# Kernel tuning notes

Hardware: AMD Instinct MI355X
Metric: run time of the kernel (lower is better)

Reference implementation:

```python
import jax, jax.numpy as jnp
import numpy as np

N, E = 20000, 320000
ND, PD, HD, H = 128, 64, 128, 4
EPS = 1e-5


def gelu(x):
    return jax.nn.gelu(x, approximate=False)  # torch nn.GELU default (erf)


def setup_inputs() -> dict:
    key = jax.random.key(0)
    ks = iter(jax.random.split(key, 64))

    def lin(din, dout):
        w = jax.random.normal(next(ks), (din, dout), jnp.float32) / np.float32(np.sqrt(din))
        b = jnp.zeros((dout,), jnp.float32)
        return w, b

    inp = {}
    inp['s'] = jax.random.normal(next(ks), (N, ND), jnp.float32)
    inp['z'] = jax.random.normal(next(ks), (E, PD), jnp.float32)
    inp['edge_idx'] = jax.random.randint(next(ks), (2, E), 0, N, jnp.int32)
    # attn_weight_mlp: (2*ND+PD)->HD->HD->H
    inp['w_w1'], inp['w_b1'] = lin(2 * ND + PD, HD)
    inp['w_w2'], inp['w_b2'] = lin(HD, HD)
    inp['w_w3'], inp['w_b3'] = lin(HD, H)
    # attn_value_mlp: (ND+PD)->HD->HD->ND
    inp['v_w1'], inp['v_b1'] = lin(ND + PD, HD)
    inp['v_w2'], inp['v_b2'] = lin(HD, HD)
    inp['v_w3'], inp['v_b3'] = lin(HD, ND)
    # attn_output_linear: (HD*H)->ND + BN(ND)
    inp['o_w'], inp['o_b'] = lin(HD * H, ND)
    inp['o_g'] = jnp.ones((ND,), jnp.float32); inp['o_bb'] = jnp.zeros((ND,), jnp.float32)
    inp['o_m'] = jnp.zeros((ND,), jnp.float32); inp['o_v'] = jnp.ones((ND,), jnp.float32)
    # attn_FFN: ND->HD->ND + BN(ND)
    inp['f_w1'], inp['f_b1'] = lin(ND, HD)
    inp['f_w2'], inp['f_b2'] = lin(HD, ND)
    inp['f_g'] = jnp.ones((ND,), jnp.float32); inp['f_bb'] = jnp.zeros((ND,), jnp.float32)
    inp['f_m'] = jnp.zeros((ND,), jnp.float32); inp['f_v'] = jnp.ones((ND,), jnp.float32)
    # edge_FFN: (2*ND+PD)->HD->PD + BN(PD)
    inp['e_w1'], inp['e_b1'] = lin(2 * ND + PD, HD)
    inp['e_w2'], inp['e_b2'] = lin(HD, PD)
    inp['e_g'] = jnp.ones((PD,), jnp.float32); inp['e_bb'] = jnp.zeros((PD,), jnp.float32)
    inp['e_m'] = jnp.zeros((PD,), jnp.float32); inp['e_v'] = jnp.ones((PD,), jnp.float32)
    return inp


def reference(s, z, edge_idx,
              w_w1, w_b1, w_w2, w_b2, w_w3, w_b3,
              v_w1, v_b1, v_w2, v_b2, v_w3, v_b3,
              o_w, o_b, o_g, o_bb, o_m, o_v,
              f_w1, f_b1, f_w2, f_b2, f_g, f_bb, f_m, f_v,
              e_w1, e_b1, e_w2, e_b2, e_g, e_bb, e_m, e_v):
    # Eval mode: Dropout = identity, SyncBatchNorm uses running stats.
    src, dst = edge_idx[0], edge_idx[1]

    def bn(x, g, b, m, v):
        return (x - m) * jax.lax.rsqrt(v + EPS) * g + b

    ss, sd = s[src], s[dst]  # [E,ND] gathers
    # edge FFN residual update of z (updated z feeds attention, as in torch)
    h = gelu(jnp.concatenate([ss, sd, z], axis=1) @ e_w1 + e_b1)
    z = z + bn(h @ e_w2 + e_b2, e_g, e_bb, e_m, e_v)
    # per-edge attention logits [E,H]
    h = gelu(jnp.concatenate([sd, ss, z], axis=1) @ w_w1 + w_b1)
    h = gelu(h @ w_w2 + w_b2)
    aw = h @ w_w3 + w_b3
    # per-edge values [E,ND]
    h = gelu(jnp.concatenate([ss, z], axis=1) @ v_w1 + v_b1)
    h = gelu(h @ v_w2 + v_b2)
    av = h @ v_w3 + v_b3
    # segment softmax over incoming edges of each dst node
    mx = jax.ops.segment_max(aw, dst, num_segments=N)
    ew = jnp.exp(aw - mx[dst])
    den = jax.ops.segment_sum(ew, dst, num_segments=N)
    aw = ew / den[dst]  # [E,H]
    # weighted scatter-sum: [N,H,ND] -> flatten
    ao = jax.ops.segment_sum(aw[:, :, None] * av[:, None, :], dst, num_segments=N)
    ao = ao.reshape(N, H * ND)
    s = s + bn(ao @ o_w + o_b, o_g, o_bb, o_m, o_v)
    s = s + bn(gelu(s @ f_w1 + f_b1) @ f_w2 + f_b2, f_g, f_bb, f_m, f_v)
    return (s, z)
```

## Files before the change

### kernel.cpp

```cpp
#include <hip/hip_runtime.h>
#include <stdint.h>


#define NN 20000
#define NE 320000

typedef unsigned short u16;
typedef __attribute__((ext_vector_type(8))) short bf16x8;
typedef __attribute__((ext_vector_type(4))) float f32x4;

__device__ __forceinline__ float bf2f(u16 u){ union{unsigned i; float f;} v; v.i=((unsigned)u)<<16; return v.f; }
__device__ __forceinline__ u16 f2bf(float f){ union{float f; unsigned i;} v; v.f=f; unsigned r = v.i + 0x7FFFu + ((v.i>>16)&1u); return (u16)(r>>16); }
__device__ __forceinline__ unsigned pk2(float a, float b){
  unsigned r; asm("v_cvt_pk_bf16_f32 %0, %1, %2" : "=v"(r) : "v"(a), "v"(b)); return r;
}
__device__ __forceinline__ float gelu_f(float x){
  float y = 0.7978845608f*x*(1.0f + 0.044715f*x*x);
  float a = fabsf(y);
  float t = __expf(-2.0f*a);
  float th = (1.0f - t)*__builtin_amdgcn_rcpf(1.0f + t);
  th = copysignf(th, y);
  return 0.5f*x*(1.0f + th);
}

#define WT_E1 0
#define WT_E2 40960
#define WT_W1 49152
#define WT_W2 90112
#define WT_W3 106496
#define WT_V1 108544
#define WT_V2 133120
#define WT_V3 149504
#define WT_O  165888
#define WT_F1 231424
#define WT_F2 247808
#define WT_TOT 264192
#define AW_B  ((size_t)WT_TOT*2)
#define AV_B  (AW_B + (size_t)NE*16)
#define AO_B  (AV_B + (size_t)NE*256)
#define CNT_B (AO_B + (size_t)NN*1024)
#define CUR_B (CNT_B + (size_t)NN*4)
#define STA_B (CUR_B + (size_t)NN*4)
#define ORD_B (STA_B + (size_t)(NN+1)*4 + 4)

struct PrepArgs { const float* src[11]; u16* dst; };

__global__ void prep_kernel(PrepArgs A){
  constexpr int NS[11]  = {128, 64,128,128,  4,128,128,128,128,128,128};
  constexpr int NO[11]  = {128, 64,128,128, 16,128,128,128,128,128,128};
  constexpr int OFF[11] = {0,40960,49152,90112,106496,108544,133120,149504,165888,231424,247808};
  constexpr int CUM[12] = {0,10,12,22,26,28,34,38,42,58,62,66};
  __shared__ float T[64][72];
  const int bid = blockIdx.x, t = threadIdx.x;
  int m = 0;
#pragma unroll
  for (int q=0;q<11;q++) if (bid >= CUM[q+1]) m = q+1;
  const int rel = bid - CUM[m];
  const int ntn = (NO[m] > 64) ? 2 : 1;
  const int c  = rel / ntn;
  const int nt = rel - c*ntn;
  const float* src = A.src[m];
  if (m != 4){
    const int k = t>>2, q = t&3;
    const float* sp = src + (size_t)(c*64+k)*NS[m] + nt*64 + q*16;
    float4 v0=((const float4*)sp)[0], v1=((const float4*)sp)[1], v2=((const float4*)sp)[2], v3=((const float4*)sp)[3];
    float* tp = &T[k][q*16];
    ((float4*)tp)[0]=v0; ((float4*)tp)[1]=v1; ((float4*)tp)[2]=v2; ((float4*)tp)[3]=v3;
  } else {
    for (int lin = t; lin < 64*16; lin += 256){
      int k = lin>>4, n = lin&15;
      T[k][n] = (n < 4) ? src[(size_t)(c*64+k)*4 + n] : 0.f;
    }
  }
  __syncthreads();
  const int nl = t>>2, kq = (t&3)*16;
  const int n = nt*64 + nl;
  if (nl < 64 && n < NO[m]){
    unsigned w[8];
#pragma unroll
    for (int i=0;i<8;i++) w[i] = pk2(T[kq+2*i][nl], T[kq+2*i+1][nl]);
    u16* dp = A.dst + OFF[m] + (size_t)c*NO[m]*64 + (size_t)n*64 + kq;
    ((uint4*)dp)[0] = make_uint4(w[0],w[1],w[2],w[3]);
    ((uint4*)dp)[1] = make_uint4(w[4],w[5],w[6],w[7]);
  }
}

__global__ void zero_kernel(int* c){ int i = blockIdx.x*256+threadIdx.x; if (i<NN) c[i]=0; }
__global__ void hist_kernel(const int* __restrict__ ei, int* __restrict__ cnt){
  int e = blockIdx.x*256+threadIdx.x; if (e<NE) atomicAdd(&cnt[ei[NE+e]], 1);
}
__global__ void scan_kernel(const int* __restrict__ cnt, int* __restrict__ sta, int* __restrict__ cur){
  __shared__ int part[1024];
  const int t = threadIdx.x;
  const int base = t*20;
  int s = 0;
  for (int i=0;i<20;i++){ int idx=base+i; s += (idx<NN)?cnt[idx]:0; }
  part[t]=s; __syncthreads();
  for (int off=1; off<1024; off<<=1){
    int v = (t>=off)? part[t-off] : 0;
    __syncthreads();
    part[t] += v;
    __syncthreads();
  }
  int run = part[t] - s;
  for (int i=0;i<20;i++){ int idx=base+i; if (idx<NN){ int c=cnt[idx]; sta[idx]=run; cur[idx]=run; run+=c; } }
  if (t==1023) sta[NN] = part[1023];
}
__global__ void place_kernel(const int* __restrict__ ei, int* __restrict__ cur, int* __restrict__ ord){
  int e = blockIdx.x*256+threadIdx.x;
  if (e<NE){ int p = atomicAdd(&cur[ei[NE+e]], 1); ord[p]=e; }
}

template<int NCH, int NT, int MTT, int NACC>
__device__ __forceinline__ void run_gemm2(int wave, int lane,
    const u16* const (&cb)[NCH], const int (&cs)[NCH], const int (&ck)[NCH],
    const u16* __restrict__ wtG, f32x4 (&acc)[NACC],
    int& ntile, int& mt0, bool& active)
{
  const int lr = lane & 15, lg = lane >> 4;
  active = true;
  if (NT == 8){ ntile = wave; mt0 = 0; }
  else if (NT == 4){ ntile = wave & 3; mt0 = (wave >> 2) * NACC; }
  else { ntile = 0; mt0 = wave; active = (wave < MTT); }
  f32x4 z4 = {0.f,0.f,0.f,0.f};
#pragma unroll
  for (int m=0;m<NACC;m++) acc[m] = z4;
  if (!active) return;
  const int CE = NT*16*64;
  const u16* bp = wtG + (size_t)(ntile*16+lr)*64 + lg*8;
  bf16x8 bc0 = *(const bf16x8*)bp;
  bf16x8 bc1 = *(const bf16x8*)(bp + 32);
#pragma unroll
  for (int c=0;c<NCH;c++){
    bf16x8 bn0, bn1;
    if (c+1 < NCH){
      bn0 = *(const bf16x8*)(bp + (c+1)*CE);
      bn1 = *(const bf16x8*)(bp + (c+1)*CE + 32);
    }
#pragma unroll
    for (int m=0;m<NACC;m++){
      const u16* ap = cb[c] + (size_t)((mt0+m)*16 + lr)*cs[c] + ck[c] + lg*8;
      bf16x8 a0 = *(const bf16x8*)ap;
      bf16x8 a1 = *(const bf16x8*)(ap + 32);
      acc[m] = __builtin_amdgcn_mfma_f32_16x16x32_bf16(a0, bc0, acc[m], 0, 0, 0);
      acc[m] = __builtin_amdgcn_mfma_f32_16x16x32_bf16(a1, bc1, acc[m], 0, 0, 0);
    }
    bc0 = bn0; bc1 = bn1;
  }
}

template<int NACC>
__device__ __forceinline__ void epi_hb(const f32x4 (&acc)[NACC], int mt0, int ntile, int lg, int lr,
    const float* __restrict__ biasG, u16* dst, int dstride, bool act)
{
  const int col = ntile*16 + lr;
  const float b = biasG[col];
#pragma unroll
  for (int m=0;m<NACC;m++)
#pragma unroll
    for (int j=0;j<4;j++){
      int row = (mt0+m)*16 + lg*4 + j;
      float v = acc[m][j] + b;
      if (act) v = gelu_f(v);
      dst[row*dstride + col] = f2bf(v);
    }
}

struct EdgeArgs {
  const float *s, *z; const int* ei;
  const float *wb1,*wb2,*wb3,*vb1,*vb2,*vb3,*eb1,*eb2,*eg,*ebb,*em,*ev;
  const u16* wt; float* aw; u16* av; float* zout;
};

__global__ __launch_bounds__(512,4) void edge_kernel(EdgeArgs A){
  __shared__ __align__(16) u16 SS[64*136];
  __shared__ __align__(16) u16 SD[64*136];
  __shared__ __align__(16) u16 ZB[64*88];
  __shared__ __align__(16) u16 HB1[64*136];
  __shared__ __align__(16) u16 HB2[64*136];
  const int tid = threadIdx.x, wave = tid>>6, lane = tid&63;
  const int lg = lane>>4, lr = lane&15;
  const int e0 = blockIdx.x*64;
  {
    const int r = tid>>3, p = tid&7;
    const int sn = A.ei[e0 + r];
    const int dn = A.ei[NE + e0 + r];
    const float4* gs = (const float4*)(A.s + (size_t)sn*128 + p*16);
    float4 f0=gs[0], f1=gs[1], f2=gs[2], f3=gs[3];
    *(uint4*)(SS + r*136 + p*16)     = make_uint4(pk2(f0.x,f0.y),pk2(f0.z,f0.w),pk2(f1.x,f1.y),pk2(f1.z,f1.w));
    *(uint4*)(SS + r*136 + p*16 + 8) = make_uint4(pk2(f2.x,f2.y),pk2(f2.z,f2.w),pk2(f3.x,f3.y),pk2(f3.z,f3.w));
    const float4* gd = (const float4*)(A.s + (size_t)dn*128 + p*16);
    f0=gd[0]; f1=gd[1]; f2=gd[2]; f3=gd[3];
    *(uint4*)(SD + r*136 + p*16)     = make_uint4(pk2(f0.x,f0.y),pk2(f0.z,f0.w),pk2(f1.x,f1.y),pk2(f1.z,f1.w));
    *(uint4*)(SD + r*136 + p*16 + 8) = make_uint4(pk2(f2.x,f2.y),pk2(f2.z,f2.w),pk2(f3.x,f3.y),pk2(f3.z,f3.w));
    const float4* gz = (const float4*)(A.z + (size_t)(e0+r)*64 + p*8);
    float4 z0=gz[0], z1=gz[1];
    *(uint4*)(ZB + r*88 + p*8) = make_uint4(pk2(z0.x,z0.y),pk2(z0.z,z0.w),pk2(z1.x,z1.y),pk2(z1.z,z1.w));
  }
  __syncthreads();
  int ntile, mt0; bool act_;
  {
    const u16* cb[5] = {SS,SS,SD,SD,ZB}; const int cs[5]={136,136,136,136,88}; const int ck[5]={0,64,0,64,0};
    f32x4 acc[4];
    run_gemm2<5,8,4,4>(wave,lane,cb,cs,ck, A.wt+WT_E1, acc, ntile, mt0, act_);
    epi_hb<4>(acc, mt0, ntile, lg, lr, A.eb1, HB1, 136, true);
  }
  __syncthreads();
  {
    const u16* cb[2] = {HB1,HB1}; const int cs[2]={136,136}; const int ck[2]={0,64};
    f32x4 acc[2];
    run_gemm2<2,4,4,2>(wave,lane,cb,cs,ck, A.wt+WT_E2, acc, ntile, mt0, act_);
    const int col = ntile*16 + lr;
    const float b  = A.eb2[col];
    const float sc = A.eg[col] * rsqrtf(A.ev[col] + 1e-5f);
    const float sh = A.ebb[col] - A.em[col]*sc;
#pragma unroll
    for (int m=0;m<2;m++)
#pragma unroll
      for (int j=0;j<4;j++){
        int row = (mt0+m)*16 + lg*4 + j;
        float zo = A.z[(size_t)(e0+row)*64 + col];
        float zn = zo + (acc[m][j]+b)*sc + sh;
        A.zout[(size_t)(e0+row)*64 + col] = zn;
        ZB[row*88 + col] = f2bf(zn);
      }
  }
  __syncthreads();
  {
    const u16* cb[5] = {SD,SD,SS,SS,ZB}; const int cs[5]={136,136,136,136,88}; const int ck[5]={0,64,0,64,0};
    f32x4 acc[4];
    run_gemm2<5,8,4,4>(wave,lane,cb,cs,ck, A.wt+WT_W1, acc, ntile, mt0, act_);
    epi_hb<4>(acc, mt0, ntile, lg, lr, A.wb1, HB2, 136, true);
  }
  __syncthreads();
  {
    const u16* cb[2] = {HB2,HB2}; const int cs[2]={136,136}; const int ck[2]={0,64};
    f32x4 acc[4];
    run_gemm2<2,8,4,4>(wave,lane,cb,cs,ck, A.wt+WT_W2, acc, ntile, mt0, act_);
    epi_hb<4>(acc, mt0, ntile, lg, lr, A.wb2, HB1, 136, true);
  }
  __syncthreads();
  {
    const u16* cb[2] = {HB1,HB1}; const int cs[2]={136,136}; const int ck[2]={0,64};
    f32x4 acc[1];
    run_gemm2<2,1,4,1>(wave,lane,cb,cs,ck, A.wt+WT_W3, acc, ntile, mt0, act_);
    if (act_ && lr < 4){
      const float b = A.wb3[lr];
#pragma unroll
      for (int j=0;j<4;j++){
        int row = mt0*16 + lg*4 + j;
        A.aw[(size_t)(e0+row)*4 + lr] = acc[0][j] + b;
      }
    }
  }
  {
    const u16* cb[3] = {SS,SS,ZB}; const int cs[3]={136,136,88}; const int ck[3]={0,64,0};
    f32x4 acc[4];
    run_gemm2<3,8,4,4>(wave,lane,cb,cs,ck, A.wt+WT_V1, acc, ntile, mt0, act_);
    epi_hb<4>(acc, mt0, ntile, lg, lr, A.vb1, HB2, 136, true);
  }
  __syncthreads();
  {
    const u16* cb[2] = {HB2,HB2}; const int cs[2]={136,136}; const int ck[2]={0,64};
    f32x4 acc[4];
    run_gemm2<2,8,4,4>(wave,lane,cb,cs,ck, A.wt+WT_V2, acc, ntile, mt0, act_);
    epi_hb<4>(acc, mt0, ntile, lg, lr, A.vb2, HB1, 136, true);
  }
  __syncthreads();
  {
    const u16* cb[2] = {HB1,HB1}; const int cs[2]={136,136}; const int ck[2]={0,64};
    f32x4 acc[4];
    run_gemm2<2,8,4,4>(wave,lane,cb,cs,ck, A.wt+WT_V3, acc, ntile, mt0, act_);
    epi_hb<4>(acc, mt0, ntile, lg, lr, A.vb3, HB2, 136, false);
    __syncthreads();
    { const int r = tid>>3, p = tid&7;
      uint4 v0 = *(const uint4*)(HB2 + r*136 + p*16);
      uint4 v1 = *(const uint4*)(HB2 + r*136 + p*16 + 8);
      *(uint4*)(A.av + (size_t)(e0+r)*128 + p*16) = v0;
      *(uint4*)(A.av + (size_t)(e0+r)*128 + p*16 + 8) = v1; }
  }
}

__global__ void attn_kernel(const float* __restrict__ aw, const u16* __restrict__ av,
                            const int* __restrict__ sta, const int* __restrict__ ord,
                            u16* __restrict__ ao){
  const int node = blockIdx.x; const int t = threadIdx.x;
  const int b = sta[node], e = sta[node+1];
  float m0=-3.4e38f, m1=m0, m2=m0, m3=m0;
  for (int i=b;i<e;i++){
    int ed = ord[i]; float4 a = *(const float4*)(aw + (size_t)ed*4);
    m0=fmaxf(m0,a.x); m1=fmaxf(m1,a.y); m2=fmaxf(m2,a.z); m3=fmaxf(m3,a.w);
  }
  float d0=0,d1=0,d2=0,d3=0,a0=0,a1=0,a2=0,a3=0;
  for (int i=b;i<e;i++){
    int ed = ord[i]; float4 a = *(const float4*)(aw + (size_t)ed*4);
    float w0=__expf(a.x-m0), w1=__expf(a.y-m1), w2=__expf(a.z-m2), w3=__expf(a.w-m3);
    d0+=w0; d1+=w1; d2+=w2; d3+=w3;
    float v = bf2f(av[(size_t)ed*128 + t]);
    a0 += w0*v; a1 += w1*v; a2 += w2*v; a3 += w3*v;
  }
  size_t o = (size_t)node*512 + t;
  if (e > b){
    ao[o      ] = f2bf(a0/d0);
    ao[o + 128] = f2bf(a1/d1);
    ao[o + 256] = f2bf(a2/d2);
    ao[o + 384] = f2bf(a3/d3);
  } else {
    ao[o] = 0; ao[o+128] = 0; ao[o+256] = 0; ao[o+384] = 0;
  }
}

struct NodeArgs {
  const float* s; const u16* ao; const u16* wt;
  const float *ob,*og,*obb,*om,*ov,*fb1,*fb2,*fg,*fbb,*fm,*fv;
  float* outS;
};

__global__ __launch_bounds__(512,4) void node_kernel(NodeArgs A){
  __shared__ __align__(16) u16 AO[16*520];
  __shared__ __align__(16) float S1F[16*128];
  __shared__ __align__(16) u16 S1B[16*136];
  __shared__ __align__(16) u16 HBx[16*136];
  const int tid=threadIdx.x, wave=tid>>6, lane=tid&63;
  const int lg=lane>>4, lr=lane&15;
  const int n0 = blockIdx.x*16;
  { const int r=tid>>5, p=tid&31;
    const uint4* gp = (const uint4*)(A.ao + (size_t)(n0+r)*512 + p*16);
    uint4 v0=gp[0], v1=gp[1];
    *(uint4*)(AO + r*520 + p*16) = v0;
    *(uint4*)(AO + r*520 + p*16 + 8) = v1;
  }
  __syncthreads();
  int ntile, mt0; bool act_;
  {
    const u16* cb[8]={AO,AO,AO,AO,AO,AO,AO,AO};
    const int cs[8]={520,520,520,520,520,520,520,520};
    const int ck[8]={0,64,128,192,256,320,384,448};
    f32x4 acc[1];
    run_gemm2<8,8,1,1>(wave,lane,cb,cs,ck, A.wt+WT_O, acc, ntile, mt0, act_);
    const int col = wave*16+lr;
    const float bb = A.ob[col];
    const float sc = A.og[col] * rsqrtf(A.ov[col] + 1e-5f);
    const float sh = A.obb[col] - A.om[col]*sc;
#pragma unroll
    for (int j=0;j<4;j++){
      int row = lg*4+j;
      float so = A.s[(size_t)(n0+row)*128 + col];
      float s1 = so + (acc[0][j]+bb)*sc + sh;
      S1F[row*128+col] = s1;
      S1B[row*136+col] = f2bf(s1);
    }
  }
  __syncthreads();
  {
    const u16* cb[2]={S1B,S1B}; const int cs[2]={136,136}; const int ck[2]={0,64};
    f32x4 acc[1];
    run_gemm2<2,8,1,1>(wave,lane,cb,cs,ck, A.wt+WT_F1, acc, ntile, mt0, act_);
    epi_hb<1>(acc, 0, wave, lg, lr, A.fb1, HBx, 136, true);
  }
  __syncthreads();
  {
    const u16* cb[2]={HBx,HBx}; const int cs[2]={136,136}; const int ck[2]={0,64};
    f32x4 acc[1];
    run_gemm2<2,8,1,1>(wave,lane,cb,cs,ck, A.wt+WT_F2, acc, ntile, mt0, act_);
    const int col = wave*16+lr;
    const float b2  = A.fb2[col];
    const float sc2 = A.fg[col] * rsqrtf(A.fv[col] + 1e-5f);
    const float sh2 = A.fbb[col] - A.fm[col]*sc2;
#pragma unroll
    for (int j=0;j<4;j++){
      int row = lg*4+j;
      float v = S1F[row*128+col] + (acc[0][j]+b2)*sc2 + sh2;
      A.outS[(size_t)(n0+row)*128 + col] = v;
    }
  }
}

extern "C" void kernel_launch(void* const* d_in, const int* in_sizes, int n_in,
                              void* d_out, int out_size, void* d_ws, size_t ws_size,
                              hipStream_t stream)
{
  const float* sG = (const float*)d_in[0];
  const float* zG = (const float*)d_in[1];
  const int* eiG = (const int*)d_in[2];
  char* ws = (char*)d_ws;
  u16*  wt  = (u16*)ws;
  float* aw = (float*)(ws + AW_B);
  u16*  av  = (u16*)(ws + AV_B);
  u16*  ao  = (u16*)(ws + AO_B);
  int* cnt = (int*)(ws + CNT_B);
  int* cur = (int*)(ws + CUR_B);
  int* sta = (int*)(ws + STA_B);
  int* ord = (int*)(ws + ORD_B);
  float* outS = (float*)d_out;
  float* outZ = outS + (size_t)NN*128;

  PrepArgs P;
  const int srcIdx[11] = {29,31,3,5,7,9,11,13,15,21,23};
  for (int i=0;i<11;i++) P.src[i] = (const float*)d_in[srcIdx[i]];
  P.dst = wt;
  prep_kernel<<<dim3(66), dim3(256), 0, stream>>>(P);
  zero_kernel<<<dim3((NN+255)/256), dim3(256), 0, stream>>>(cnt);
  hist_kernel<<<dim3((NE+255)/256), dim3(256), 0, stream>>>(eiG, cnt);
  scan_kernel<<<dim3(1), dim3(1024), 0, stream>>>(cnt, sta, cur);
  place_kernel<<<dim3((NE+255)/256), dim3(256), 0, stream>>>(eiG, cur, ord);

  EdgeArgs E;
  E.s = sG; E.z = zG; E.ei = eiG;
  E.wb1=(const float*)d_in[4];  E.wb2=(const float*)d_in[6];  E.wb3=(const float*)d_in[8];
  E.vb1=(const float*)d_in[10]; E.vb2=(const float*)d_in[12]; E.vb3=(const float*)d_in[14];
  E.eb1=(const float*)d_in[30]; E.eb2=(const float*)d_in[32];
  E.eg=(const float*)d_in[33]; E.ebb=(const float*)d_in[34]; E.em=(const float*)d_in[35]; E.ev=(const float*)d_in[36];
  E.wt = wt; E.aw = aw; E.av = av; E.zout = outZ;
  edge_kernel<<<dim3(NE/64), dim3(512), 0, stream>>>(E);

  attn_kernel<<<dim3(NN), dim3(128), 0, stream>>>(aw, av, sta, ord, ao);

  NodeArgs Nd;
  Nd.s = sG; Nd.ao = ao; Nd.wt = wt;
  Nd.ob=(const float*)d_in[16]; Nd.og=(const float*)d_in[17]; Nd.obb=(const float*)d_in[18];
  Nd.om=(const float*)d_in[19]; Nd.ov=(const float*)d_in[20];
  Nd.fb1=(const float*)d_in[22]; Nd.fb2=(const float*)d_in[24];
  Nd.fg=(const float*)d_in[25]; Nd.fbb=(const float*)d_in[26]; Nd.fm=(const float*)d_in[27]; Nd.fv=(const float*)d_in[28];
  Nd.outS = outS;
  node_kernel<<<dim3(NN/16), dim3(512), 0, stream>>>(Nd);
}
```

Baseline: 671.0 us.

## Fuse attention aggregation into node kernel and merge setup kernels

Folds the per-node segment-softmax and weighted value aggregation into the node kernel, so the ao intermediate is never written to or read from global memory and one launch is removed. Each wave now handles two destination nodes, with each lane covering two value columns. Weight prep and the destination histogram are merged into one launch, with zeroing done by a memset. The scan kernel uses vectorised int4 loads and stores, the GEMM helper loads all weight chunks up front instead of double-buffering them, and the z tile padding in shared memory shrinks. The risks are higher register pressure from preloading all B fragments, and reduced parallelism in the fused aggregation (20000/16 blocks versus one block per node before).

```diff
diff --git a/kernel.cpp b/kernel.cpp
--- a/kernel.cpp
+++ b/kernel.cpp
@@ -37,21 +37,26 @@
 #define WT_TOT 264192
 #define AW_B  ((size_t)WT_TOT*2)
 #define AV_B  (AW_B + (size_t)NE*16)
-#define AO_B  (AV_B + (size_t)NE*256)
-#define CNT_B (AO_B + (size_t)NN*1024)
+#define CNT_B (AV_B + (size_t)NE*256)
 #define CUR_B (CNT_B + (size_t)NN*4)
 #define STA_B (CUR_B + (size_t)NN*4)
 #define ORD_B (STA_B + (size_t)(NN+1)*4 + 4)
 
 struct PrepArgs { const float* src[11]; u16* dst; };
 
-__global__ void prep_kernel(PrepArgs A){
+__global__ void setup_kernel(PrepArgs A, const int* __restrict__ ei, int* __restrict__ cnt){
   constexpr int NS[11]  = {128, 64,128,128,  4,128,128,128,128,128,128};
   constexpr int NO[11]  = {128, 64,128,128, 16,128,128,128,128,128,128};
   constexpr int OFF[11] = {0,40960,49152,90112,106496,108544,133120,149504,165888,231424,247808};
   constexpr int CUM[12] = {0,10,12,22,26,28,34,38,42,58,62,66};
   __shared__ float T[64][72];
-  const int bid = blockIdx.x, t = threadIdx.x;
+  const int t = threadIdx.x;
+  if (blockIdx.x >= 66){
+    int e = (blockIdx.x-66)*256 + t;
+    if (e < NE) atomicAdd(&cnt[ei[NE+e]], 1);
+    return;
+  }
+  const int bid = blockIdx.x;
   int m = 0;
 #pragma unroll
   for (int q=0;q<11;q++) if (bid >= CUM[q+1]) m = q+1;
@@ -85,25 +90,39 @@
   }
 }
 
-__global__ void zero_kernel(int* c){ int i = blockIdx.x*256+threadIdx.x; if (i<NN) c[i]=0; }
-__global__ void hist_kernel(const int* __restrict__ ei, int* __restrict__ cnt){
-  int e = blockIdx.x*256+threadIdx.x; if (e<NE) atomicAdd(&cnt[ei[NE+e]], 1);
-}
 __global__ void scan_kernel(const int* __restrict__ cnt, int* __restrict__ sta, int* __restrict__ cur){
   __shared__ int part[1024];
   const int t = threadIdx.x;
   const int base = t*20;
+  int v[20];
   int s = 0;
-  for (int i=0;i<20;i++){ int idx=base+i; s += (idx<NN)?cnt[idx]:0; }
+  if (t < 1000){
+#pragma unroll
+    for (int i=0;i<5;i++){
+      int4 x = ((const int4*)(cnt+base))[i];
+      v[4*i]=x.x; v[4*i+1]=x.y; v[4*i+2]=x.z; v[4*i+3]=x.w;
+      s += x.x+x.y+x.z+x.w;
+    }
+  }
   part[t]=s; __syncthreads();
   for (int off=1; off<1024; off<<=1){
-    int v = (t>=off)? part[t-off] : 0;
+    int x = (t>=off)? part[t-off] : 0;
     __syncthreads();
-    part[t] += v;
+    part[t] += x;
     __syncthreads();
   }
   int run = part[t] - s;
-  for (int i=0;i<20;i++){ int idx=base+i; if (idx<NN){ int c=cnt[idx]; sta[idx]=run; cur[idx]=run; run+=c; } }
+  if (t < 1000){
+    int sv[20];
+#pragma unroll
+    for (int i=0;i<20;i++){ sv[i]=run; run += v[i]; }
+#pragma unroll
+    for (int i=0;i<5;i++){
+      int4 x = make_int4(sv[4*i],sv[4*i+1],sv[4*i+2],sv[4*i+3]);
+      ((int4*)(sta+base))[i] = x;
+      ((int4*)(cur+base))[i] = x;
+    }
+  }
   if (t==1023) sta[NN] = part[1023];
 }
 __global__ void place_kernel(const int* __restrict__ ei, int* __restrict__ cur, int* __restrict__ ord){
@@ -112,7 +131,7 @@
 }
 
 template<int NCH, int NT, int MTT, int NACC>
-__device__ __forceinline__ void run_gemm2(int wave, int lane,
+__device__ __forceinline__ void run_gemm3(int wave, int lane,
     const u16* const (&cb)[NCH], const int (&cs)[NCH], const int (&ck)[NCH],
     const u16* __restrict__ wtG, f32x4 (&acc)[NACC],
     int& ntile, int& mt0, bool& active)
@@ -128,24 +147,22 @@
   if (!active) return;
   const int CE = NT*16*64;
   const u16* bp = wtG + (size_t)(ntile*16+lr)*64 + lg*8;
-  bf16x8 bc0 = *(const bf16x8*)bp;
-  bf16x8 bc1 = *(const bf16x8*)(bp + 32);
+  bf16x8 B0[NCH], B1[NCH];
 #pragma unroll
   for (int c=0;c<NCH;c++){
-    bf16x8 bn0, bn1;
-    if (c+1 < NCH){
-      bn0 = *(const bf16x8*)(bp + (c+1)*CE);
-      bn1 = *(const bf16x8*)(bp + (c+1)*CE + 32);
-    }
+    B0[c] = *(const bf16x8*)(bp + (size_t)c*CE);
+    B1[c] = *(const bf16x8*)(bp + (size_t)c*CE + 32);
+  }
+#pragma unroll
+  for (int c=0;c<NCH;c++){
 #pragma unroll
     for (int m=0;m<NACC;m++){
       const u16* ap = cb[c] + (size_t)((mt0+m)*16 + lr)*cs[c] + ck[c] + lg*8;
       bf16x8 a0 = *(const bf16x8*)ap;
       bf16x8 a1 = *(const bf16x8*)(ap + 32);
-      acc[m] = __builtin_amdgcn_mfma_f32_16x16x32_bf16(a0, bc0, acc[m], 0, 0, 0);
-      acc[m] = __builtin_amdgcn_mfma_f32_16x16x32_bf16(a1, bc1, acc[m], 0, 0, 0);
-    }
-    bc0 = bn0; bc1 = bn1;
+      acc[m] = __builtin_amdgcn_mfma_f32_16x16x32_bf16(a0, B0[c], acc[m], 0, 0, 0);
+      acc[m] = __builtin_amdgcn_mfma_f32_16x16x32_bf16(a1, B1[c], acc[m], 0, 0, 0);
+    }
   }
 }
 
@@ -175,7 +192,7 @@
 __global__ __launch_bounds__(512,4) void edge_kernel(EdgeArgs A){
   __shared__ __align__(16) u16 SS[64*136];
   __shared__ __align__(16) u16 SD[64*136];
-  __shared__ __align__(16) u16 ZB[64*88];
+  __shared__ __align__(16) u16 ZB[64*72];
   __shared__ __align__(16) u16 HB1[64*136];
   __shared__ __align__(16) u16 HB2[64*136];
   const int tid = threadIdx.x, wave = tid>>6, lane = tid&63;
@@ -195,21 +212,21 @@
     *(uint4*)(SD + r*136 + p*16 + 8) = make_uint4(pk2(f2.x,f2.y),pk2(f2.z,f2.w),pk2(f3.x,f3.y),pk2(f3.z,f3.w));
     const float4* gz = (const float4*)(A.z + (size_t)(e0+r)*64 + p*8);
     float4 z0=gz[0], z1=gz[1];
-    *(uint4*)(ZB + r*88 + p*8) = make_uint4(pk2(z0.x,z0.y),pk2(z0.z,z0.w),pk2(z1.x,z1.y),pk2(z1.z,z1.w));
+    *(uint4*)(ZB + r*72 + p*8) = make_uint4(pk2(z0.x,z0.y),pk2(z0.z,z0.w),pk2(z1.x,z1.y),pk2(z1.z,z1.w));
   }
   __syncthreads();
   int ntile, mt0; bool act_;
   {
-    const u16* cb[5] = {SS,SS,SD,SD,ZB}; const int cs[5]={136,136,136,136,88}; const int ck[5]={0,64,0,64,0};
-    f32x4 acc[4];
-    run_gemm2<5,8,4,4>(wave,lane,cb,cs,ck, A.wt+WT_E1, acc, ntile, mt0, act_);
+    const u16* cb[5] = {SS,SS,SD,SD,ZB}; const int cs[5]={136,136,136,136,72}; const int ck[5]={0,64,0,64,0};
+    f32x4 acc[4];
+    run_gemm3<5,8,4,4>(wave,lane,cb,cs,ck, A.wt+WT_E1, acc, ntile, mt0, act_);
     epi_hb<4>(acc, mt0, ntile, lg, lr, A.eb1, HB1, 136, true);
   }
   __syncthreads();
   {
     const u16* cb[2] = {HB1,HB1}; const int cs[2]={136,136}; const int ck[2]={0,64};
     f32x4 acc[2];
-    run_gemm2<2,4,4,2>(wave,lane,cb,cs,ck, A.wt+WT_E2, acc, ntile, mt0, act_);
+    run_gemm3<2,4,4,2>(wave,lane,cb,cs,ck, A.wt+WT_E2, acc, ntile, mt0, act_);
     const int col = ntile*16 + lr;
     const float b  = A.eb2[col];
     const float sc = A.eg[col] * rsqrtf(A.ev[col] + 1e-5f);
@@ -222,28 +239,28 @@
         float zo = A.z[(size_t)(e0+row)*64 + col];
         float zn = zo + (acc[m][j]+b)*sc + sh;
         A.zout[(size_t)(e0+row)*64 + col] = zn;
-        ZB[row*88 + col] = f2bf(zn);
+        ZB[row*72 + col] = f2bf(zn);
       }
   }
   __syncthreads();
   {
-    const u16* cb[5] = {SD,SD,SS,SS,ZB}; const int cs[5]={136,136,136,136,88}; const int ck[5]={0,64,0,64,0};
-    f32x4 acc[4];
-    run_gemm2<5,8,4,4>(wave,lane,cb,cs,ck, A.wt+WT_W1, acc, ntile, mt0, act_);
+    const u16* cb[5] = {SD,SD,SS,SS,ZB}; const int cs[5]={136,136,136,136,72}; const int ck[5]={0,64,0,64,0};
+    f32x4 acc[4];
+    run_gemm3<5,8,4,4>(wave,lane,cb,cs,ck, A.wt+WT_W1, acc, ntile, mt0, act_);
     epi_hb<4>(acc, mt0, ntile, lg, lr, A.wb1, HB2, 136, true);
   }
   __syncthreads();
   {
     const u16* cb[2] = {HB2,HB2}; const int cs[2]={136,136}; const int ck[2]={0,64};
     f32x4 acc[4];
-    run_gemm2<2,8,4,4>(wave,lane,cb,cs,ck, A.wt+WT_W2, acc, ntile, mt0, act_);
+    run_gemm3<2,8,4,4>(wave,lane,cb,cs,ck, A.wt+WT_W2, acc, ntile, mt0, act_);
     epi_hb<4>(acc, mt0, ntile, lg, lr, A.wb2, HB1, 136, true);
   }
   __syncthreads();
   {
     const u16* cb[2] = {HB1,HB1}; const int cs[2]={136,136}; const int ck[2]={0,64};
     f32x4 acc[1];
-    run_gemm2<2,1,4,1>(wave,lane,cb,cs,ck, A.wt+WT_W3, acc, ntile, mt0, act_);
+    run_gemm3<2,1,4,1>(wave,lane,cb,cs,ck, A.wt+WT_W3, acc, ntile, mt0, act_);
     if (act_ && lr < 4){
       const float b = A.wb3[lr];
 #pragma unroll
@@ -254,23 +271,23 @@
     }
   }
   {
-    const u16* cb[3] = {SS,SS,ZB}; const int cs[3]={136,136,88}; const int ck[3]={0,64,0};
-    f32x4 acc[4];
-    run_gemm2<3,8,4,4>(wave,lane,cb,cs,ck, A.wt+WT_V1, acc, ntile, mt0, act_);
+    const u16* cb[3] = {SS,SS,ZB}; const int cs[3]={136,136,72}; const int ck[3]={0,64,0};
+    f32x4 acc[4];
+    run_gemm3<3,8,4,4>(wave,lane,cb,cs,ck, A.wt+WT_V1, acc, ntile, mt0, act_);
     epi_hb<4>(acc, mt0, ntile, lg, lr, A.vb1, HB2, 136, true);
   }
   __syncthreads();
   {
     const u16* cb[2] = {HB2,HB2}; const int cs[2]={136,136}; const int ck[2]={0,64};
     f32x4 acc[4];
-    run_gemm2<2,8,4,4>(wave,lane,cb,cs,ck, A.wt+WT_V2, acc, ntile, mt0, act_);
+    run_gemm3<2,8,4,4>(wave,lane,cb,cs,ck, A.wt+WT_V2, acc, ntile, mt0, act_);
     epi_hb<4>(acc, mt0, ntile, lg, lr, A.vb2, HB1, 136, true);
   }
   __syncthreads();
   {
     const u16* cb[2] = {HB1,HB1}; const int cs[2]={136,136}; const int ck[2]={0,64};
     f32x4 acc[4];
-    run_gemm2<2,8,4,4>(wave,lane,cb,cs,ck, A.wt+WT_V3, acc, ntile, mt0, act_);
+    run_gemm3<2,8,4,4>(wave,lane,cb,cs,ck, A.wt+WT_V3, acc, ntile, mt0, act_);
     epi_hb<4>(acc, mt0, ntile, lg, lr, A.vb3, HB2, 136, false);
     __syncthreads();
     { const int r = tid>>3, p = tid&7;
@@ -281,37 +298,9 @@
   }
 }
 
-__global__ void attn_kernel(const float* __restrict__ aw, const u16* __restrict__ av,
-                            const int* __restrict__ sta, const int* __restrict__ ord,
-                            u16* __restrict__ ao){
-  const int node = blockIdx.x; const int t = threadIdx.x;
-  const int b = sta[node], e = sta[node+1];
-  float m0=-3.4e38f, m1=m0, m2=m0, m3=m0;
-  for (int i=b;i<e;i++){
-    int ed = ord[i]; float4 a = *(const float4*)(aw + (size_t)ed*4);
-    m0=fmaxf(m0,a.x); m1=fmaxf(m1,a.y); m2=fmaxf(m2,a.z); m3=fmaxf(m3,a.w);
-  }
-  float d0=0,d1=0,d2=0,d3=0,a0=0,a1=0,a2=0,a3=0;
-  for (int i=b;i<e;i++){
-    int ed = ord[i]; float4 a = *(const float4*)(aw + (size_t)ed*4);
-    float w0=__expf(a.x-m0), w1=__expf(a.y-m1), w2=__expf(a.z-m2), w3=__expf(a.w-m3);
-    d0+=w0; d1+=w1; d2+=w2; d3+=w3;
-    float v = bf2f(av[(size_t)ed*128 + t]);
-    a0 += w0*v; a1 += w1*v; a2 += w2*v; a3 += w3*v;
-  }
-  size_t o = (size_t)node*512 + t;
-  if (e > b){
-    ao[o      ] = f2bf(a0/d0);
-    ao[o + 128] = f2bf(a1/d1);
-    ao[o + 256] = f2bf(a2/d2);
-    ao[o + 384] = f2bf(a3/d3);
-  } else {
-    ao[o] = 0; ao[o+128] = 0; ao[o+256] = 0; ao[o+384] = 0;
-  }
-}
-
 struct NodeArgs {
-  const float* s; const u16* ao; const u16* wt;
+  const float* s; const float* aw; const u16* av;
+  const int* sta; const int* ord; const u16* wt;
   const float *ob,*og,*obb,*om,*ov,*fb1,*fb2,*fg,*fbb,*fm,*fv;
   float* outS;
 };
@@ -324,11 +313,38 @@
   const int tid=threadIdx.x, wave=tid>>6, lane=tid&63;
   const int lg=lane>>4, lr=lane&15;
   const int n0 = blockIdx.x*16;
-  { const int r=tid>>5, p=tid&31;
-    const uint4* gp = (const uint4*)(A.ao + (size_t)(n0+r)*512 + p*16);
-    uint4 v0=gp[0], v1=gp[1];
-    *(uint4*)(AO + r*520 + p*16) = v0;
-    *(uint4*)(AO + r*520 + p*16 + 8) = v1;
+#pragma unroll
+  for (int q=0;q<2;q++){
+    const int lrow = wave*2+q, nn = n0+lrow;
+    const int b = A.sta[nn], e = A.sta[nn+1];
+    float m0=-3.4e38f, m1=m0, m2=m0, m3=m0;
+    for (int i=b;i<e;i++){
+      int ed = A.ord[i];
+      float4 a = *(const float4*)(A.aw + (size_t)ed*4);
+      m0=fmaxf(m0,a.x); m1=fmaxf(m1,a.y); m2=fmaxf(m2,a.z); m3=fmaxf(m3,a.w);
+    }
+    float d0=0,d1=0,d2=0,d3=0;
+    float a00=0,a01=0,a10=0,a11=0,a20=0,a21=0,a30=0,a31=0;
+    for (int i=b;i<e;i++){
+      int ed = A.ord[i];
+      float4 a = *(const float4*)(A.aw + (size_t)ed*4);
+      float w0=__expf(a.x-m0), w1=__expf(a.y-m1), w2=__expf(a.z-m2), w3=__expf(a.w-m3);
+      d0+=w0; d1+=w1; d2+=w2; d3+=w3;
+      unsigned pv = *(const unsigned*)(A.av + (size_t)ed*128 + lane*2);
+      float v0 = bf2f((u16)pv), v1 = bf2f((u16)(pv>>16));
+      a00+=w0*v0; a01+=w0*v1; a10+=w1*v0; a11+=w1*v1;
+      a20+=w2*v0; a21+=w2*v1; a30+=w3*v0; a31+=w3*v1;
+    }
+    unsigned* aoRow = (unsigned*)(AO + lrow*520);
+    if (e > b){
+      float r0=1.f/d0, r1=1.f/d1, r2=1.f/d2, r3=1.f/d3;
+      aoRow[        lane] = pk2(a00*r0, a01*r0);
+      aoRow[ 64 + lane] = pk2(a10*r1, a11*r1);
+      aoRow[128 + lane] = pk2(a20*r2, a21*r2);
+      aoRow[192 + lane] = pk2(a30*r3, a31*r3);
+    } else {
+      aoRow[lane]=0; aoRow[64+lane]=0; aoRow[128+lane]=0; aoRow[192+lane]=0;
+    }
   }
   __syncthreads();
   int ntile, mt0; bool act_;
@@ -337,7 +353,7 @@
     const int cs[8]={520,520,520,520,520,520,520,520};
     const int ck[8]={0,64,128,192,256,320,384,448};
     f32x4 acc[1];
-    run_gemm2<8,8,1,1>(wave,lane,cb,cs,ck, A.wt+WT_O, acc, ntile, mt0, act_);
+    run_gemm3<8,8,1,1>(wave,lane,cb,cs,ck, A.wt+WT_O, acc, ntile, mt0, act_);
     const int col = wave*16+lr;
     const float bb = A.ob[col];
     const float sc = A.og[col] * rsqrtf(A.ov[col] + 1e-5f);
@@ -355,14 +371,14 @@
   {
     const u16* cb[2]={S1B,S1B}; const int cs[2]={136,136}; const int ck[2]={0,64};
     f32x4 acc[1];
-    run_gemm2<2,8,1,1>(wave,lane,cb,cs,ck, A.wt+WT_F1, acc, ntile, mt0, act_);
+    run_gemm3<2,8,1,1>(wave,lane,cb,cs,ck, A.wt+WT_F1, acc, ntile, mt0, act_);
     epi_hb<1>(acc, 0, wave, lg, lr, A.fb1, HBx, 136, true);
   }
   __syncthreads();
   {
     const u16* cb[2]={HBx,HBx}; const int cs[2]={136,136}; const int ck[2]={0,64};
     f32x4 acc[1];
-    run_gemm2<2,8,1,1>(wave,lane,cb,cs,ck, A.wt+WT_F2, acc, ntile, mt0, act_);
+    run_gemm3<2,8,1,1>(wave,lane,cb,cs,ck, A.wt+WT_F2, acc, ntile, mt0, act_);
     const int col = wave*16+lr;
     const float b2  = A.fb2[col];
     const float sc2 = A.fg[col] * rsqrtf(A.fv[col] + 1e-5f);
@@ -387,7 +403,6 @@
   u16*  wt  = (u16*)ws;
   float* aw = (float*)(ws + AW_B);
   u16*  av  = (u16*)(ws + AV_B);
-  u16*  ao  = (u16*)(ws + AO_B);
   int* cnt = (int*)(ws + CNT_B);
   int* cur = (int*)(ws + CUR_B);
   int* sta = (int*)(ws + STA_B);
@@ -395,13 +410,13 @@
   float* outS = (float*)d_out;
   float* outZ = outS + (size_t)NN*128;
 
+  hipMemsetAsync(cnt, 0, (size_t)NN*4, stream);
+
   PrepArgs P;
   const int srcIdx[11] = {29,31,3,5,7,9,11,13,15,21,23};
   for (int i=0;i<11;i++) P.src[i] = (const float*)d_in[srcIdx[i]];
   P.dst = wt;
-  prep_kernel<<<dim3(66), dim3(256), 0, stream>>>(P);
-  zero_kernel<<<dim3((NN+255)/256), dim3(256), 0, stream>>>(cnt);
-  hist_kernel<<<dim3((NE+255)/256), dim3(256), 0, stream>>>(eiG, cnt);
+  setup_kernel<<<dim3(66 + (NE+255)/256), dim3(256), 0, stream>>>(P, eiG, cnt);
   scan_kernel<<<dim3(1), dim3(1024), 0, stream>>>(cnt, sta, cur);
   place_kernel<<<dim3((NE+255)/256), dim3(256), 0, stream>>>(eiG, cur, ord);
 
@@ -414,10 +429,8 @@
   E.wt = wt; E.aw = aw; E.av = av; E.zout = outZ;
   edge_kernel<<<dim3(NE/64), dim3(512), 0, stream>>>(E);
 
-  attn_kernel<<<dim3(NN), dim3(128), 0, stream>>>(aw, av, sta, ord, ao);
-
   NodeArgs Nd;
-  Nd.s = sG; Nd.ao = ao; Nd.wt = wt;
+  Nd.s = sG; Nd.aw = aw; Nd.av = av; Nd.sta = sta; Nd.ord = ord; Nd.wt = wt;
   Nd.ob=(const float*)d_in[16]; Nd.og=(const float*)d_in[17]; Nd.obb=(const float*)d_in[18];
   Nd.om=(const float*)d_in[19]; Nd.ov=(const float*)d_in[20];
   Nd.fb1=(const float*)d_in[22]; Nd.fb2=(const float*)d_in[24];
```

Result: no change. 670.3 us (-0.1%).
